# Performance work log

Hardware: AMD Instinct MI355X
Metric: run time of the kernel (lower is better)

The kernel has to match this reference:

```python
import jax, jax.numpy as jnp
import numpy as np

N, IN_DIM, HIDDEN, CLASSES, HEADS, E = 4096, 256, 512, 256, 4, 131072
HD = IN_DIM // HEADS


def setup_inputs() -> dict:
    key = jax.random.key(0)
    ks = jax.random.split(key, 16)
    s = 0.02
    x = jax.random.normal(ks[0], (N, IN_DIM), dtype=jnp.float32)
    edge_index = jax.random.randint(ks[1], (2, E), 0, N, dtype=jnp.int64)
    return {
        "x": x,
        "edge_index": edge_index,
        # GCNConv 1: in_dim -> hidden
        "gcn1_w": jax.random.normal(ks[2], (IN_DIM, HIDDEN), dtype=jnp.float32) * s,
        "gcn1_b": jnp.zeros((HIDDEN,), dtype=jnp.float32),
        # GCNConv 2: hidden -> hidden
        "gcn2_w": jax.random.normal(ks[3], (HIDDEN, HIDDEN), dtype=jnp.float32) * s,
        "gcn2_b": jnp.zeros((HIDDEN,), dtype=jnp.float32),
        # final Linear hidden -> classes
        "lin_w": jax.random.normal(ks[4], (HIDDEN, CLASSES), dtype=jnp.float32) * s,
        "lin_b": jnp.zeros((CLASSES,), dtype=jnp.float32),
        # MultiheadAttention packed in-projection (q,k,v) and out-projection
        "in_proj_w": jax.random.normal(ks[5], (3 * IN_DIM, IN_DIM), dtype=jnp.float32) * s,
        "in_proj_b": jnp.zeros((3 * IN_DIM,), dtype=jnp.float32),
        "out_proj_w": jax.random.normal(ks[6], (IN_DIM, IN_DIM), dtype=jnp.float32) * s,
        "out_proj_b": jnp.zeros((IN_DIM,), dtype=jnp.float32),
        # project: in_dim -> classes
        "proj_w": jax.random.normal(ks[7], (IN_DIM, CLASSES), dtype=jnp.float32) * s,
        "proj_b": jnp.zeros((CLASSES,), dtype=jnp.float32),
    }


def gcn_conv(x, src, dst, norm, w, b):
    # PyG GCNConv: transform, then normalized scatter-add aggregation
    h = x @ w                                   # [N+?, F] -> use gathered below
    msg = h[src] * norm[:, None]                # [E+N, F]
    out = jax.ops.segment_sum(msg, dst, num_segments=N)
    return out + b


def mha(x, in_proj_w, in_proj_b, out_proj_w, out_proj_b):
    qkv = x @ in_proj_w.T + in_proj_b           # [N, 3*IN_DIM]
    q, k, v = jnp.split(qkv, 3, axis=-1)
    # [N, IN_DIM] -> [HEADS, N, HD]
    q = q.reshape(N, HEADS, HD).transpose(1, 0, 2)
    k = k.reshape(N, HEADS, HD).transpose(1, 0, 2)
    v = v.reshape(N, HEADS, HD).transpose(1, 0, 2)
    scores = jnp.einsum("hqd,hkd->hqk", q, k) / jnp.sqrt(jnp.float32(HD))
    attn = jax.nn.softmax(scores, axis=-1)      # [HEADS, N, N]
    o = jnp.einsum("hqk,hkd->hqd", attn, v)     # [HEADS, N, HD]
    o = o.transpose(1, 0, 2).reshape(N, IN_DIM)
    return o @ out_proj_w.T + out_proj_b


def reference(x, edge_index, gcn1_w, gcn1_b, gcn2_w, gcn2_b, lin_w, lin_b,
              in_proj_w, in_proj_b, out_proj_w, out_proj_b, proj_w, proj_b):
    # --- GCN normalization with self-loops (computed once, shared by both convs) ---
    loop = jnp.arange(N, dtype=edge_index.dtype)
    src = jnp.concatenate([edge_index[0], loop])  # [E+N]
    dst = jnp.concatenate([edge_index[1], loop])
    deg = jax.ops.segment_sum(jnp.ones_like(dst, dtype=jnp.float32), dst, num_segments=N)
    dinv = jnp.where(deg > 0, jax.lax.rsqrt(deg), 0.0)
    norm = dinv[src] * dinv[dst]                  # [E+N]

    # --- GNN branch ---
    h = jax.nn.relu(gcn_conv(x, src, dst, norm, gcn1_w, gcn1_b))
    h = jax.nn.relu(gcn_conv(h, src, dst, norm, gcn2_w, gcn2_b))
    x_gnn = h @ lin_w + lin_b                     # [N, CLASSES]

    # --- Transformer branch ---
    x_tf = mha(x, in_proj_w, in_proj_b, out_proj_w, out_proj_b)
    x_proj = x_tf @ proj_w + proj_b               # [N, CLASSES]

    return jax.nn.relu(x_gnn + x_proj)
```

## Files before the change

### kernel.cpp

```cpp
#include <hip/hip_runtime.h>
#include <hip/hip_bf16.h>

#define N_NODES 4096
#define IN_DIM  256
#define HIDDEN  512
#define CLASSES 256
#define HEADS   4
#define HD      64
#define NEDGE   131072
#define NMASK   (N_NODES - 1)

typedef __attribute__((ext_vector_type(8))) short bf16x8_t;
typedef __attribute__((ext_vector_type(4))) float f32x4_t;

__device__ inline ushort f2bf(float f) {
    union { float f; uint u; } v; v.f = f;
    uint r = v.u + 0x7FFF + ((v.u >> 16) & 1);
    return (ushort)(r >> 16);
}
__device__ inline float bf2f(ushort u) {
    union { uint u; float f; } v; v.u = (uint)u << 16; return v.f;
}

__global__ void zero_i_k(int* __restrict__ p, int n) {
    int i = blockIdx.x * 256 + threadIdx.x;
    if (i < n) p[i] = 0;
}
__global__ void hist_k(const int* __restrict__ dst, int* __restrict__ cnt) {
    int i = blockIdx.x * 256 + threadIdx.x;
    if (i < NEDGE) atomicAdd(&cnt[dst[i] & NMASK], 1);
}
__global__ __launch_bounds__(256) void scan_k(const int* __restrict__ cnt,
                                              int* __restrict__ rowptr,
                                              float* __restrict__ dinv) {
    __shared__ int part[256];
    const int t = threadIdx.x;
    const int base = t * 16;
    int local[16];
    int s = 0;
    #pragma unroll
    for (int u = 0; u < 16; ++u) { local[u] = cnt[base + u]; s += local[u]; }
    part[t] = s;
    __syncthreads();
    if (t == 0) {
        int acc = 0;
        for (int i = 0; i < 256; ++i) { int v = part[i]; part[i] = acc; acc += v; }
    }
    __syncthreads();
    int acc = part[t];
    #pragma unroll
    for (int u = 0; u < 16; ++u) {
        rowptr[base + u] = acc;
        acc += local[u];
        dinv[base + u] = rsqrtf((float)local[u] + 1.0f);
    }
    if (t == 255) rowptr[N_NODES] = acc;
}
__global__ void scatter_k(const int* __restrict__ src, const int* __restrict__ dst,
                          const int* __restrict__ rowptr, int* __restrict__ tail,
                          int* __restrict__ ssrc) {
    int e = blockIdx.x * 256 + threadIdx.x;
    if (e >= NEDGE) return;
    int d = dst[e] & NMASK;
    int pos = rowptr[d] + atomicAdd(&tail[d], 1);
    ssrc[pos] = src[e] & NMASK;
}

__global__ void split_k(const float* __restrict__ in, ushort* __restrict__ hi,
                        ushort* __restrict__ lo, int n4) {
    int i = blockIdx.x * 256 + threadIdx.x;
    if (i >= n4) return;
    float4 v = ((const float4*)in)[i];
    ushort4 h, l;
    h.x = f2bf(v.x); l.x = f2bf(v.x - bf2f(h.x));
    h.y = f2bf(v.y); l.y = f2bf(v.y - bf2f(h.y));
    h.z = f2bf(v.z); l.z = f2bf(v.z - bf2f(h.z));
    h.w = f2bf(v.w); l.w = f2bf(v.w - bf2f(h.w));
    ((ushort4*)hi)[i] = h;
    ((ushort4*)lo)[i] = l;
}

__global__ __launch_bounds__(256) void tsplit_k(const float* __restrict__ W,
                                                ushort* __restrict__ th,
                                                ushort* __restrict__ tl,
                                                int K, int N) {
    __shared__ float T[64][68];
    const int k0 = blockIdx.x * 64, n0 = blockIdx.y * 64;
    const int t = threadIdx.x;
    {
        const int r = t >> 2, q = (t & 3) * 16;
        const float* src = W + (size_t)(k0 + r) * N + n0 + q;
        #pragma unroll
        for (int i = 0; i < 4; ++i)
            *(float4*)&T[r][q + i * 4] = *(const float4*)(src + i * 4);
    }
    __syncthreads();
    const int n = t >> 2, kq = (t & 3) * 16;
    ushort hh[16], ll[16];
    #pragma unroll
    for (int i = 0; i < 16; ++i) {
        float v = T[kq + i][n];
        ushort h = f2bf(v);
        hh[i] = h; ll[i] = f2bf(v - bf2f(h));
    }
    ushort* ph = th + (size_t)(n0 + n) * K + k0 + kq;
    ushort* pl = tl + (size_t)(n0 + n) * K + k0 + kq;
    #pragma unroll
    for (int i = 0; i < 16; ++i) { ph[i] = hh[i]; pl[i] = ll[i]; }
}

template<int MODE>
__global__ __launch_bounds__(256) void gemm_sp_k(
    const ushort* __restrict__ Ah, const ushort* __restrict__ Al,
    const ushort* __restrict__ Bh, const ushort* __restrict__ Bl,
    const float* __restrict__ bias, const float* src,
    void* o1, void* o2, int M, int N, int K)
{
    __shared__ ushort AsH[64][32], AsL[64][32], BsH[64][32], BsL[64][32];
    const int tid = threadIdx.x;
    const int w = tid >> 6, lane = tid & 63, g = lane >> 4, c = lane & 15;
    const int wr = w >> 1, wc = w & 1;
    const int m0 = blockIdx.x * 64, n0 = blockIdx.y * 64;
    const int sr = tid >> 2, sq = (tid & 3) * 8;

    f32x4_t acc[2][2];
    #pragma unroll
    for (int i = 0; i < 2; ++i)
        #pragma unroll
        for (int j = 0; j < 2; ++j) { acc[i][j][0]=0.f; acc[i][j][1]=0.f; acc[i][j][2]=0.f; acc[i][j][3]=0.f; }

    for (int k0 = 0; k0 < K; k0 += 32) {
        __syncthreads();
        *(bf16x8_t*)&AsH[sr][sq] = *(const bf16x8_t*)(Ah + (size_t)(m0 + sr) * K + k0 + sq);
        *(bf16x8_t*)&AsL[sr][sq] = *(const bf16x8_t*)(Al + (size_t)(m0 + sr) * K + k0 + sq);
        *(bf16x8_t*)&BsH[sr][sq] = *(const bf16x8_t*)(Bh + (size_t)(n0 + sr) * K + k0 + sq);
        *(bf16x8_t*)&BsL[sr][sq] = *(const bf16x8_t*)(Bl + (size_t)(n0 + sr) * K + k0 + sq);
        __syncthreads();

        bf16x8_t aH[2], aL[2], bH[2], bL[2];
        #pragma unroll
        for (int mr = 0; mr < 2; ++mr) {
            aH[mr] = *(const bf16x8_t*)&AsH[wr * 32 + mr * 16 + c][g * 8];
            aL[mr] = *(const bf16x8_t*)&AsL[wr * 32 + mr * 16 + c][g * 8];
        }
        #pragma unroll
        for (int nr = 0; nr < 2; ++nr) {
            bH[nr] = *(const bf16x8_t*)&BsH[wc * 32 + nr * 16 + c][g * 8];
            bL[nr] = *(const bf16x8_t*)&BsL[wc * 32 + nr * 16 + c][g * 8];
        }
        #pragma unroll
        for (int mr = 0; mr < 2; ++mr)
            #pragma unroll
            for (int nr = 0; nr < 2; ++nr) {
                acc[mr][nr] = __builtin_amdgcn_mfma_f32_16x16x32_bf16(aH[mr], bH[nr], acc[mr][nr], 0, 0, 0);
                acc[mr][nr] = __builtin_amdgcn_mfma_f32_16x16x32_bf16(aH[mr], bL[nr], acc[mr][nr], 0, 0, 0);
                acc[mr][nr] = __builtin_amdgcn_mfma_f32_16x16x32_bf16(aL[mr], bH[nr], acc[mr][nr], 0, 0, 0);
            }
    }

    #pragma unroll
    for (int mr = 0; mr < 2; ++mr)
        #pragma unroll
        for (int nr = 0; nr < 2; ++nr) {
            const int col = n0 + wc * 32 + nr * 16 + c;
            #pragma unroll
            for (int j = 0; j < 4; ++j) {
                const int row = m0 + wr * 32 + mr * 16 + g * 4 + j;
                float v = acc[mr][nr][j];
                if (MODE != 3) v += bias[col];
                if (MODE == 0) {
                    ((float*)o1)[(size_t)row * N + col] = v;
                } else if (MODE == 1) {
                    v += src[(size_t)row * N + col];
                    ((float*)o1)[(size_t)row * N + col] = fmaxf(v, 0.f);
                } else if (MODE == 2 || MODE == 3) {
                    ushort h = f2bf(v);
                    ((ushort*)o1)[(size_t)row * N + col] = h;
                    ((ushort*)o2)[(size_t)row * N + col] = f2bf(v - bf2f(h));
                } else {
                    if (col < 256) v *= 0.125f;
                    ((ushort*)o1)[(size_t)row * N + col] = f2bf(v);
                }
            }
        }
}

__global__ __launch_bounds__(256) void vtrans_k(const ushort* __restrict__ qkvb,
                                                ushort* __restrict__ vt) {
    __shared__ ushort T[64][72];
    const int n0 = blockIdx.x * 64;
    const int h  = blockIdx.y;
    const int t  = threadIdx.x;
    {
        const int r = t >> 2, q = (t & 3) * 16;
        const ushort* src = qkvb + (size_t)(n0 + r) * 768 + 512 + h * 64 + q;
        *(bf16x8_t*)&T[r][q]     = *(const bf16x8_t*)(src);
        *(bf16x8_t*)&T[r][q + 8] = *(const bf16x8_t*)(src + 8);
    }
    __syncthreads();
    const int d = t >> 2, nq = (t & 3) * 16;
    ushort tmp[16];
    #pragma unroll
    for (int i = 0; i < 16; ++i) tmp[i] = T[nq + i][d];
    ushort* dst = vt + (size_t)(h * 64 + d) * 4096 + n0 + nq;
    #pragma unroll
    for (int i = 0; i < 16; ++i) dst[i] = tmp[i];
}

__global__ __launch_bounds__(64) void attn3_k(const ushort* __restrict__ qkvb,
                                              const ushort* __restrict__ vt,
                                              float* __restrict__ po0,
                                              float* __restrict__ po1,
                                              float* __restrict__ pml)
{
    __shared__ ushort Ps[16][72];

    const int q0   = blockIdx.x * 16;
    const int h    = blockIdx.y;
    const int sp   = blockIdx.z;
    const int lane = threadIdx.x;
    const int g    = lane >> 4;
    const int c    = lane & 15;

    const ushort* qp = qkvb + (size_t)(q0 + c) * 768 + h * 64;
    const bf16x8_t qf0 = *(const bf16x8_t*)(qp + g * 8);
    const bf16x8_t qf1 = *(const bf16x8_t*)(qp + g * 8 + 32);

    f32x4_t o[4];
    float m[4], l[4];
    #pragma unroll
    for (int r = 0; r < 4; ++r) {
        m[r] = -1e30f; l[r] = 0.f;
        o[r][0] = 0.f; o[r][1] = 0.f; o[r][2] = 0.f; o[r][3] = 0.f;
    }

    const ushort* kcol = qkvb + 256 + h * 64 + g * 8;
    const ushort* vrow = vt + (size_t)(h * 64 + c) * 4096 + g * 8;

    for (int kt = sp * 32; kt < sp * 32 + 32; ++kt) {
        const int kv0 = kt * 64;

        f32x4_t s[4];
        #pragma unroll
        for (int t = 0; t < 4; ++t) {
            const ushort* kr = kcol + (size_t)(kv0 + c + 16 * t) * 768;
            bf16x8_t b0 = *(const bf16x8_t*)(kr);
            bf16x8_t b1 = *(const bf16x8_t*)(kr + 32);
            f32x4_t a; a[0] = 0.f; a[1] = 0.f; a[2] = 0.f; a[3] = 0.f;
            a = __builtin_amdgcn_mfma_f32_16x16x32_bf16(qf0, b0, a, 0, 0, 0);
            a = __builtin_amdgcn_mfma_f32_16x16x32_bf16(qf1, b1, a, 0, 0, 0);
            s[t] = a;
        }

        bf16x8_t vf[4][2];
        #pragma unroll
        for (int d0 = 0; d0 < 4; ++d0) {
            const ushort* vr = vrow + (size_t)(16 * d0) * 4096 + kv0;
            vf[d0][0] = *(const bf16x8_t*)(vr);
            vf[d0][1] = *(const bf16x8_t*)(vr + 32);
        }

        #pragma unroll
        for (int r = 0; r < 4; ++r) {
            float mx = fmaxf(fmaxf(s[0][r], s[1][r]), fmaxf(s[2][r], s[3][r]));
            mx = fmaxf(mx, __shfl_xor(mx, 1));
            mx = fmaxf(mx, __shfl_xor(mx, 2));
            mx = fmaxf(mx, __shfl_xor(mx, 4));
            mx = fmaxf(mx, __shfl_xor(mx, 8));
            float mn = fmaxf(m[r], mx);
            float alpha = __expf(m[r] - mn);
            m[r] = mn;
            float p0 = __expf(s[0][r] - mn);
            float p1 = __expf(s[1][r] - mn);
            float p2 = __expf(s[2][r] - mn);
            float p3 = __expf(s[3][r] - mn);
            float sum = p0 + p1 + p2 + p3;
            sum += __shfl_xor(sum, 1);
            sum += __shfl_xor(sum, 2);
            sum += __shfl_xor(sum, 4);
            sum += __shfl_xor(sum, 8);
            l[r] = l[r] * alpha + sum;
            o[0][r] *= alpha; o[1][r] *= alpha; o[2][r] *= alpha; o[3][r] *= alpha;
            ushort* pr = &Ps[g * 4 + r][c];
            pr[0]  = f2bf(p0);
            pr[16] = f2bf(p1);
            pr[32] = f2bf(p2);
            pr[48] = f2bf(p3);
        }

        bf16x8_t pa0 = *(const bf16x8_t*)&Ps[c][g * 8];
        bf16x8_t pa1 = *(const bf16x8_t*)&Ps[c][g * 8 + 32];
        #pragma unroll
        for (int d0 = 0; d0 < 4; ++d0) {
            o[d0] = __builtin_amdgcn_mfma_f32_16x16x32_bf16(pa0, vf[d0][0], o[d0], 0, 0, 0);
            o[d0] = __builtin_amdgcn_mfma_f32_16x16x32_bf16(pa1, vf[d0][1], o[d0], 0, 0, 0);
        }
    }

    float* po = sp ? po1 : po0;
    #pragma unroll
    for (int r = 0; r < 4; ++r) {
        float* op = po + ((size_t)h * 4096 + q0 + g * 4 + r) * 64 + c;
        #pragma unroll
        for (int d0 = 0; d0 < 4; ++d0)
            op[16 * d0] = o[d0][r];
    }
    if (c == 0) {
        #pragma unroll
        for (int r = 0; r < 4; ++r) {
            size_t idx = ((size_t)(sp * 4 + h) * 4096 + q0 + g * 4 + r) * 2;
            pml[idx]     = m[r];
            pml[idx + 1] = l[r];
        }
    }
}

__global__ __launch_bounds__(256) void comb_k(const float* __restrict__ po0,
                                              const float* __restrict__ po1,
                                              const float* __restrict__ pml,
                                              ushort* __restrict__ aoh,
                                              ushort* __restrict__ aol)
{
    int idx = blockIdx.x * 256 + threadIdx.x;
    int row = idx >> 4;
    int h = row >> 12, q = row & 4095;
    int dq = (idx & 15) * 4;
    const float* a = pml + ((size_t)(0 * 4 + h) * 4096 + q) * 2;
    const float* b = pml + ((size_t)(1 * 4 + h) * 4096 + q) * 2;
    float m1 = a[0], l1 = a[1], m2 = b[0], l2 = b[1];
    float mw = fmaxf(m1, m2);
    float a1 = __expf(m1 - mw), a2 = __expf(m2 - mw);
    float inv = 1.0f / (a1 * l1 + a2 * l2);
    float4 o1 = *(const float4*)(po0 + (size_t)row * 64 + dq);
    float4 o2 = *(const float4*)(po1 + (size_t)row * 64 + dq);
    float vx = (a1 * o1.x + a2 * o2.x) * inv;
    float vy = (a1 * o1.y + a2 * o2.y) * inv;
    float vz = (a1 * o1.z + a2 * o2.z) * inv;
    float vw = (a1 * o1.w + a2 * o2.w) * inv;
    size_t oi = (size_t)q * 256 + h * 64 + dq;
    ushort4 H, L;
    H.x = f2bf(vx); L.x = f2bf(vx - bf2f(H.x));
    H.y = f2bf(vy); L.y = f2bf(vy - bf2f(H.y));
    H.z = f2bf(vz); L.z = f2bf(vz - bf2f(H.z));
    H.w = f2bf(vw); L.w = f2bf(vw - bf2f(H.w));
    *(ushort4*)(aoh + oi) = H;
    *(ushort4*)(aol + oi) = L;
}

__global__ __launch_bounds__(128) void csr_agg2_k(const ushort* __restrict__ hh,
                                                  const ushort* __restrict__ hl,
                                                  const int* __restrict__ rowptr,
                                                  const int* __restrict__ ssrc,
                                                  const float* __restrict__ dinv,
                                                  const float* __restrict__ bias,
                                                  ushort* __restrict__ oh,
                                                  ushort* __restrict__ ol) {
    __shared__ int   nbr[64];
    __shared__ float wnb[64];
    const int d = blockIdx.x;
    const int c = threadIdx.x;
    const int beg = rowptr[d], end = rowptr[d + 1];

    float4 acc = {0.f, 0.f, 0.f, 0.f};
    for (int j0 = beg; j0 < end; j0 += 64) {
        const int mcnt = min(64, end - j0);
        if (c < mcnt) {
            int s = ssrc[j0 + c];
            nbr[c] = s;
            wnb[c] = dinv[s];
        }
        __syncthreads();
        for (int u = 0; u < mcnt; ++u) {
            const int s = nbr[u];
            const float w = wnb[u];
            ushort4 vh = *(const ushort4*)(hh + (size_t)s * 512 + c * 4);
            ushort4 vl = *(const ushort4*)(hl + (size_t)s * 512 + c * 4);
            acc.x += w * (bf2f(vh.x) + bf2f(vl.x));
            acc.y += w * (bf2f(vh.y) + bf2f(vl.y));
            acc.z += w * (bf2f(vh.z) + bf2f(vl.z));
            acc.w += w * (bf2f(vh.w) + bf2f(vl.w));
        }
        __syncthreads();
    }

    const float wd = dinv[d];
    const float wd2 = wd * wd;
    ushort4 sh = *(const ushort4*)(hh + (size_t)d * 512 + c * 4);
    ushort4 sl = *(const ushort4*)(hl + (size_t)d * 512 + c * 4);
    float4 bv = *((const float4*)bias + c);
    float r0 = fmaxf(acc.x * wd + wd2 * (bf2f(sh.x) + bf2f(sl.x)) + bv.x, 0.f);
    float r1 = fmaxf(acc.y * wd + wd2 * (bf2f(sh.y) + bf2f(sl.y)) + bv.y, 0.f);
    float r2 = fmaxf(acc.z * wd + wd2 * (bf2f(sh.z) + bf2f(sl.z)) + bv.z, 0.f);
    float r3 = fmaxf(acc.w * wd + wd2 * (bf2f(sh.w) + bf2f(sl.w)) + bv.w, 0.f);
    ushort4 H, L;
    H.x = f2bf(r0); L.x = f2bf(r0 - bf2f(H.x));
    H.y = f2bf(r1); L.y = f2bf(r1 - bf2f(H.y));
    H.z = f2bf(r2); L.z = f2bf(r2 - bf2f(H.z));
    H.w = f2bf(r3); L.w = f2bf(r3 - bf2f(H.w));
    *(ushort4*)(oh + (size_t)d * 512 + c * 4) = H;
    *(ushort4*)(ol + (size_t)d * 512 + c * 4) = L;
}

extern "C" void kernel_launch(void* const* d_in, const int* in_sizes, int n_in,
                              void* d_out, int out_size, void* d_ws, size_t ws_size,
                              hipStream_t stream)
{
    const float* x          = (const float*)d_in[0];
    const int*   eidx       = (const int*)d_in[1];
    const float* gcn1_w     = (const float*)d_in[2];
    const float* gcn1_b     = (const float*)d_in[3];
    const float* gcn2_w     = (const float*)d_in[4];
    const float* gcn2_b     = (const float*)d_in[5];
    const float* lin_w      = (const float*)d_in[6];
    const float* lin_b      = (const float*)d_in[7];
    const float* in_proj_w  = (const float*)d_in[8];
    const float* in_proj_b  = (const float*)d_in[9];
    const float* out_proj_w = (const float*)d_in[10];
    const float* out_proj_b = (const float*)d_in[11];
    const float* proj_w     = (const float*)d_in[12];
    const float* proj_b     = (const float*)d_in[13];
    float* out = (float*)d_out;

    const int* esrc = eidx;
    const int* edst = eidx + NEDGE;

    char* base = (char*)d_ws;
    size_t off = 0;
    auto take = [&](size_t bytes) -> char* {
        char* p = base + off;
        off = (off + bytes + 255) & ~(size_t)255;
        return p;
    };

    int*   cnt    = (int*)take(N_NODES * 4);
    int*   tail   = (int*)take(N_NODES * 4);
    int*   rowptr = (int*)take((N_NODES + 8) * 4);
    int*   ssrc   = (int*)take(NEDGE * 4);
    float* dinv   = (float*)take(N_NODES * 4);
    float* pml    = (float*)take(2 * HEADS * N_NODES * 2 * 4);

    ushort* wreg = (ushort*)take(2 * 1024 * 1024);
    ushort* ipW_h = wreg;
    ushort* ipW_l = ipW_h + 768 * 256;
    ushort* opW_h = ipW_l + 768 * 256;
    ushort* opW_l = opW_h + 256 * 256;
    ushort* pjT_h = opW_l + 256 * 256;
    ushort* pjT_l = pjT_h + 256 * 256;
    ushort* g1T_h = wreg;
    ushort* g1T_l = g1T_h + 512 * 256;
    ushort* g2T_h = g1T_l + 512 * 256;
    ushort* g2T_l = g2T_h + 512 * 512;
    ushort* lT_h  = g2T_l + 512 * 512;
    ushort* lT_l  = lT_h + 256 * 512;

    ushort* xs_h = (ushort*)take(N_NODES * IN_DIM * 2);
    ushort* xs_l = (ushort*)take(N_NODES * IN_DIM * 2);

    char* R2 = take(8 * 1024 * 1024);
    ushort* qkvb = (ushort*)R2;
    ushort* vt   = qkvb + (size_t)N_NODES * 768;
    ushort* Ph   = (ushort*)R2;
    ushort* Pl   = Ph + (size_t)N_NODES * HIDDEN;

    char* R3 = take(8 * 1024 * 1024);
    ushort* ao_h = (ushort*)R3;
    ushort* ao_l = ao_h + (size_t)N_NODES * IN_DIM;
    ushort* xt_h = ao_l + (size_t)N_NODES * IN_DIM;
    ushort* xt_l = xt_h + (size_t)N_NODES * IN_DIM;
    ushort* Qh   = (ushort*)R3;
    ushort* Ql   = Qh + (size_t)N_NODES * HIDDEN;

    float* po0 = out;
    float* po1 = (float*)xt_h;

    zero_i_k<<<(2 * N_NODES + 255) / 256, 256, 0, stream>>>(cnt, 2 * N_NODES);
    hist_k<<<(NEDGE + 255) / 256, 256, 0, stream>>>(edst, cnt);
    scan_k<<<1, 256, 0, stream>>>(cnt, rowptr, dinv);
    scatter_k<<<(NEDGE + 255) / 256, 256, 0, stream>>>(esrc, edst, rowptr, tail, ssrc);

    split_k<<<(N_NODES * IN_DIM / 4 + 255) / 256, 256, 0, stream>>>(x, xs_h, xs_l, N_NODES * IN_DIM / 4);
    split_k<<<(768 * 256 / 4 + 255) / 256, 256, 0, stream>>>(in_proj_w, ipW_h, ipW_l, 768 * 256 / 4);
    split_k<<<(256 * 256 / 4 + 255) / 256, 256, 0, stream>>>(out_proj_w, opW_h, opW_l, 256 * 256 / 4);
    tsplit_k<<<dim3(4, 4), 256, 0, stream>>>(proj_w, pjT_h, pjT_l, 256, 256);

    gemm_sp_k<4><<<dim3(64, 12), 256, 0, stream>>>(xs_h, xs_l, ipW_h, ipW_l,
        in_proj_b, nullptr, qkvb, nullptr, N_NODES, 768, 256);
    vtrans_k<<<dim3(64, 4), 256, 0, stream>>>(qkvb, vt);
    attn3_k<<<dim3(256, 4, 2), 64, 0, stream>>>(qkvb, vt, po0, po1, pml);
    comb_k<<<(HEADS * N_NODES * 16) / 256, 256, 0, stream>>>(po0, po1, pml, ao_h, ao_l);
    gemm_sp_k<2><<<dim3(64, 4), 256, 0, stream>>>(ao_h, ao_l, opW_h, opW_l,
        out_proj_b, nullptr, xt_h, xt_l, N_NODES, 256, 256);
    gemm_sp_k<0><<<dim3(64, 4), 256, 0, stream>>>(xt_h, xt_l, pjT_h, pjT_l,
        proj_b, nullptr, out, nullptr, N_NODES, 256, 256);

    tsplit_k<<<dim3(4, 8), 256, 0, stream>>>(gcn1_w, g1T_h, g1T_l, 256, 512);
    tsplit_k<<<dim3(8, 8), 256, 0, stream>>>(gcn2_w, g2T_h, g2T_l, 512, 512);
    tsplit_k<<<dim3(8, 4), 256, 0, stream>>>(lin_w, lT_h, lT_l, 512, 256);

    gemm_sp_k<3><<<dim3(64, 8), 256, 0, stream>>>(xs_h, xs_l, g1T_h, g1T_l,
        nullptr, nullptr, Ph, Pl, N_NODES, HIDDEN, IN_DIM);
    csr_agg2_k<<<N_NODES, 128, 0, stream>>>(Ph, Pl, rowptr, ssrc, dinv, gcn1_b, Qh, Ql);
    gemm_sp_k<3><<<dim3(64, 8), 256, 0, stream>>>(Qh, Ql, g2T_h, g2T_l,
        nullptr, nullptr, Ph, Pl, N_NODES, HIDDEN, HIDDEN);
    csr_agg2_k<<<N_NODES, 128, 0, stream>>>(Ph, Pl, rowptr, ssrc, dinv, gcn2_b, Qh, Ql);

    gemm_sp_k<1><<<dim3(64, 4), 256, 0, stream>>>(Qh, Ql, lT_h, lT_l,
        lin_b, out, out, nullptr, N_NODES, CLASSES, HIDDEN);
}
```

Before: 375.7 us.

## Split attention KV range three ways with register double-buffered K prefetch

The flash-attention kernel now splits the 64 KV tiles into three chunks instead of two. That raises the block count for more parallelism across CUs, and a three-way combine kernel merges the partial results. Inside the loop, K fragments for the next tile are loaded into a second register set while the current tile is computed, so global load latency is hidden. Intermediate buffers are remapped to hold the third partial output. The cost is more registers per thread, tempered by a launch_bounds occupancy hint, plus extra combine traffic.

After: 378.2 us. Within noise of the previous version (+0.7%).

```diff
diff --git a/kernel.cpp b/kernel.cpp
--- a/kernel.cpp
+++ b/kernel.cpp
@@ -207,17 +207,88 @@
     for (int i = 0; i < 16; ++i) dst[i] = tmp[i];
 }
 
-__global__ __launch_bounds__(64) void attn3_k(const ushort* __restrict__ qkvb,
-                                              const ushort* __restrict__ vt,
-                                              float* __restrict__ po0,
-                                              float* __restrict__ po1,
-                                              float* __restrict__ pml)
+#define PF_K(KB, KTIDX)                                                        \
+    {                                                                          \
+        const int kk = (KTIDX);                                                \
+        const size_t b = (size_t)(kk * 64 + c) * 768;                          \
+        KB[0][0] = *(const bf16x8_t*)(kcol + b);                               \
+        KB[0][1] = *(const bf16x8_t*)(kcol + b + 32);                          \
+        KB[1][0] = *(const bf16x8_t*)(kcol + b + 16 * 768);                    \
+        KB[1][1] = *(const bf16x8_t*)(kcol + b + 16 * 768 + 32);               \
+        KB[2][0] = *(const bf16x8_t*)(kcol + b + 32 * 768);                    \
+        KB[2][1] = *(const bf16x8_t*)(kcol + b + 32 * 768 + 32);               \
+        KB[3][0] = *(const bf16x8_t*)(kcol + b + 48 * 768);                    \
+        KB[3][1] = *(const bf16x8_t*)(kcol + b + 48 * 768 + 32);               \
+    }
+
+#define ATTN_TILE(KB, KT)                                                      \
+    {                                                                          \
+        const int kv0 = (KT) * 64;                                             \
+        bf16x8_t vf[4][2];                                                     \
+        _Pragma("unroll")                                                      \
+        for (int d0 = 0; d0 < 4; ++d0) {                                       \
+            const ushort* vr = vrow + (size_t)(16 * d0) * 4096 + kv0;          \
+            vf[d0][0] = *(const bf16x8_t*)(vr);                                \
+            vf[d0][1] = *(const bf16x8_t*)(vr + 32);                           \
+        }                                                                      \
+        f32x4_t s[4];                                                          \
+        _Pragma("unroll")                                                      \
+        for (int t = 0; t < 4; ++t) {                                          \
+            f32x4_t a; a[0] = 0.f; a[1] = 0.f; a[2] = 0.f; a[3] = 0.f;         \
+            a = __builtin_amdgcn_mfma_f32_16x16x32_bf16(qf0, KB[t][0], a, 0, 0, 0); \
+            a = __builtin_amdgcn_mfma_f32_16x16x32_bf16(qf1, KB[t][1], a, 0, 0, 0); \
+            s[t] = a;                                                          \
+        }                                                                      \
+        _Pragma("unroll")                                                      \
+        for (int r = 0; r < 4; ++r) {                                          \
+            float mx = fmaxf(fmaxf(s[0][r], s[1][r]), fmaxf(s[2][r], s[3][r]));\
+            mx = fmaxf(mx, __shfl_xor(mx, 1));                                 \
+            mx = fmaxf(mx, __shfl_xor(mx, 2));                                 \
+            mx = fmaxf(mx, __shfl_xor(mx, 4));                                 \
+            mx = fmaxf(mx, __shfl_xor(mx, 8));                                 \
+            float mn = fmaxf(m[r], mx);                                        \
+            float alpha = __expf(m[r] - mn);                                   \
+            m[r] = mn;                                                         \
+            float p0 = __expf(s[0][r] - mn);                                   \
+            float p1 = __expf(s[1][r] - mn);                                   \
+            float p2 = __expf(s[2][r] - mn);                                   \
+            float p3 = __expf(s[3][r] - mn);                                   \
+            float sum = p0 + p1 + p2 + p3;                                     \
+            sum += __shfl_xor(sum, 1);                                         \
+            sum += __shfl_xor(sum, 2);                                         \
+            sum += __shfl_xor(sum, 4);                                         \
+            sum += __shfl_xor(sum, 8);                                         \
+            l[r] = l[r] * alpha + sum;                                         \
+            o[0][r] *= alpha; o[1][r] *= alpha; o[2][r] *= alpha; o[3][r] *= alpha; \
+            ushort* pr = &Ps[g * 4 + r][c];                                    \
+            pr[0]  = f2bf(p0);                                                 \
+            pr[16] = f2bf(p1);                                                 \
+            pr[32] = f2bf(p2);                                                 \
+            pr[48] = f2bf(p3);                                                 \
+        }                                                                      \
+        bf16x8_t pa0 = *(const bf16x8_t*)&Ps[c][g * 8];                        \
+        bf16x8_t pa1 = *(const bf16x8_t*)&Ps[c][g * 8 + 32];                   \
+        _Pragma("unroll")                                                      \
+        for (int d0 = 0; d0 < 4; ++d0) {                                       \
+            o[d0] = __builtin_amdgcn_mfma_f32_16x16x32_bf16(pa0, vf[d0][0], o[d0], 0, 0, 0); \
+            o[d0] = __builtin_amdgcn_mfma_f32_16x16x32_bf16(pa1, vf[d0][1], o[d0], 0, 0, 0); \
+        }                                                                      \
+    }
+
+__global__ __launch_bounds__(64, 3) void attn4_k(const ushort* __restrict__ qkvb,
+                                                 const ushort* __restrict__ vt,
+                                                 float* __restrict__ po0,
+                                                 float* __restrict__ po1,
+                                                 float* __restrict__ po2,
+                                                 float* __restrict__ pml)
 {
     __shared__ ushort Ps[16][72];
 
     const int q0   = blockIdx.x * 16;
     const int h    = blockIdx.y;
     const int sp   = blockIdx.z;
+    const int kt_beg = sp * 22;
+    const int kt_end = min(64, kt_beg + 22);
     const int lane = threadIdx.x;
     const int g    = lane >> 4;
     const int c    = lane & 15;
@@ -237,67 +308,23 @@
     const ushort* kcol = qkvb + 256 + h * 64 + g * 8;
     const ushort* vrow = vt + (size_t)(h * 64 + c) * 4096 + g * 8;
 
-    for (int kt = sp * 32; kt < sp * 32 + 32; ++kt) {
-        const int kv0 = kt * 64;
-
-        f32x4_t s[4];
-        #pragma unroll
-        for (int t = 0; t < 4; ++t) {
-            const ushort* kr = kcol + (size_t)(kv0 + c + 16 * t) * 768;
-            bf16x8_t b0 = *(const bf16x8_t*)(kr);
-            bf16x8_t b1 = *(const bf16x8_t*)(kr + 32);
-            f32x4_t a; a[0] = 0.f; a[1] = 0.f; a[2] = 0.f; a[3] = 0.f;
-            a = __builtin_amdgcn_mfma_f32_16x16x32_bf16(qf0, b0, a, 0, 0, 0);
-            a = __builtin_amdgcn_mfma_f32_16x16x32_bf16(qf1, b1, a, 0, 0, 0);
-            s[t] = a;
-        }
-
-        bf16x8_t vf[4][2];
-        #pragma unroll
-        for (int d0 = 0; d0 < 4; ++d0) {
-            const ushort* vr = vrow + (size_t)(16 * d0) * 4096 + kv0;
-            vf[d0][0] = *(const bf16x8_t*)(vr);
-            vf[d0][1] = *(const bf16x8_t*)(vr + 32);
-        }
-
-        #pragma unroll
-        for (int r = 0; r < 4; ++r) {
-            float mx = fmaxf(fmaxf(s[0][r], s[1][r]), fmaxf(s[2][r], s[3][r]));
-            mx = fmaxf(mx, __shfl_xor(mx, 1));
-            mx = fmaxf(mx, __shfl_xor(mx, 2));
-            mx = fmaxf(mx, __shfl_xor(mx, 4));
-            mx = fmaxf(mx, __shfl_xor(mx, 8));
-            float mn = fmaxf(m[r], mx);
-            float alpha = __expf(m[r] - mn);
-            m[r] = mn;
-            float p0 = __expf(s[0][r] - mn);
-            float p1 = __expf(s[1][r] - mn);
-            float p2 = __expf(s[2][r] - mn);
-            float p3 = __expf(s[3][r] - mn);
-            float sum = p0 + p1 + p2 + p3;
-            sum += __shfl_xor(sum, 1);
-            sum += __shfl_xor(sum, 2);
-            sum += __shfl_xor(sum, 4);
-            sum += __shfl_xor(sum, 8);
-            l[r] = l[r] * alpha + sum;
-            o[0][r] *= alpha; o[1][r] *= alpha; o[2][r] *= alpha; o[3][r] *= alpha;
-            ushort* pr = &Ps[g * 4 + r][c];
-            pr[0]  = f2bf(p0);
-            pr[16] = f2bf(p1);
-            pr[32] = f2bf(p2);
-            pr[48] = f2bf(p3);
-        }
-
-        bf16x8_t pa0 = *(const bf16x8_t*)&Ps[c][g * 8];
-        bf16x8_t pa1 = *(const bf16x8_t*)&Ps[c][g * 8 + 32];
-        #pragma unroll
-        for (int d0 = 0; d0 < 4; ++d0) {
-            o[d0] = __builtin_amdgcn_mfma_f32_16x16x32_bf16(pa0, vf[d0][0], o[d0], 0, 0, 0);
-            o[d0] = __builtin_amdgcn_mfma_f32_16x16x32_bf16(pa1, vf[d0][1], o[d0], 0, 0, 0);
-        }
-    }
-
-    float* po = sp ? po1 : po0;
+    bf16x8_t kbA[4][2], kbB[4][2];
+    PF_K(kbA, kt_beg)
+
+    for (int kt = kt_beg; kt < kt_end; kt += 2) {
+        {
+            const int ktn = kt + 1;
+            PF_K(kbB, ktn)
+        }
+        ATTN_TILE(kbA, kt)
+        {
+            const int ktn2 = min(kt + 2, kt_end - 1);
+            PF_K(kbA, ktn2)
+        }
+        ATTN_TILE(kbB, kt + 1)
+    }
+
+    float* po = (sp == 0) ? po0 : (sp == 1) ? po1 : po2;
     #pragma unroll
     for (int r = 0; r < 4; ++r) {
         float* op = po + ((size_t)h * 4096 + q0 + g * 4 + r) * 64 + c;
@@ -315,11 +342,12 @@
     }
 }
 
-__global__ __launch_bounds__(256) void comb_k(const float* __restrict__ po0,
-                                              const float* __restrict__ po1,
-                                              const float* __restrict__ pml,
-                                              ushort* __restrict__ aoh,
-                                              ushort* __restrict__ aol)
+__global__ __launch_bounds__(256) void comb3_k(const float* __restrict__ po0,
+                                               const float* __restrict__ po1,
+                                               const float* __restrict__ po2,
+                                               const float* __restrict__ pml,
+                                               ushort* __restrict__ aoh,
+                                               ushort* __restrict__ aol)
 {
     int idx = blockIdx.x * 256 + threadIdx.x;
     int row = idx >> 4;
@@ -327,16 +355,18 @@
     int dq = (idx & 15) * 4;
     const float* a = pml + ((size_t)(0 * 4 + h) * 4096 + q) * 2;
     const float* b = pml + ((size_t)(1 * 4 + h) * 4096 + q) * 2;
-    float m1 = a[0], l1 = a[1], m2 = b[0], l2 = b[1];
-    float mw = fmaxf(m1, m2);
-    float a1 = __expf(m1 - mw), a2 = __expf(m2 - mw);
-    float inv = 1.0f / (a1 * l1 + a2 * l2);
-    float4 o1 = *(const float4*)(po0 + (size_t)row * 64 + dq);
-    float4 o2 = *(const float4*)(po1 + (size_t)row * 64 + dq);
-    float vx = (a1 * o1.x + a2 * o2.x) * inv;
-    float vy = (a1 * o1.y + a2 * o2.y) * inv;
-    float vz = (a1 * o1.z + a2 * o2.z) * inv;
-    float vw = (a1 * o1.w + a2 * o2.w) * inv;
+    const float* e = pml + ((size_t)(2 * 4 + h) * 4096 + q) * 2;
+    float m0 = a[0], l0 = a[1], m1 = b[0], l1 = b[1], m2 = e[0], l2 = e[1];
+    float mw = fmaxf(fmaxf(m0, m1), m2);
+    float a0 = __expf(m0 - mw), a1 = __expf(m1 - mw), a2 = __expf(m2 - mw);
+    float inv = 1.0f / (a0 * l0 + a1 * l1 + a2 * l2);
+    float4 o0 = *(const float4*)(po0 + (size_t)row * 64 + dq);
+    float4 o1 = *(const float4*)(po1 + (size_t)row * 64 + dq);
+    float4 o2 = *(const float4*)(po2 + (size_t)row * 64 + dq);
+    float vx = (a0 * o0.x + a1 * o1.x + a2 * o2.x) * inv;
+    float vy = (a0 * o0.y + a1 * o1.y + a2 * o2.y) * inv;
+    float vz = (a0 * o0.z + a1 * o1.z + a2 * o2.z) * inv;
+    float vw = (a0 * o0.w + a1 * o1.w + a2 * o2.w) * inv;
     size_t oi = (size_t)q * 256 + h * 64 + dq;
     ushort4 H, L;
     H.x = f2bf(vx); L.x = f2bf(vx - bf2f(H.x));
@@ -437,7 +467,7 @@
     int*   rowptr = (int*)take((N_NODES + 8) * 4);
     int*   ssrc   = (int*)take(NEDGE * 4);
     float* dinv   = (float*)take(N_NODES * 4);
-    float* pml    = (float*)take(2 * HEADS * N_NODES * 2 * 4);
+    float* pml    = (float*)take(3 * HEADS * N_NODES * 2 * 4);
 
     ushort* wreg = (ushort*)take(2 * 1024 * 1024);
     ushort* ipW_h = wreg;
@@ -459,19 +489,20 @@
     char* R2 = take(8 * 1024 * 1024);
     ushort* qkvb = (ushort*)R2;
     ushort* vt   = qkvb + (size_t)N_NODES * 768;
+    ushort* ao_h = (ushort*)R2;
+    ushort* ao_l = ao_h + (size_t)N_NODES * IN_DIM;
     ushort* Ph   = (ushort*)R2;
     ushort* Pl   = Ph + (size_t)N_NODES * HIDDEN;
 
     char* R3 = take(8 * 1024 * 1024);
-    ushort* ao_h = (ushort*)R3;
-    ushort* ao_l = ao_h + (size_t)N_NODES * IN_DIM;
-    ushort* xt_h = ao_l + (size_t)N_NODES * IN_DIM;
+    float* po1 = (float*)R3;
+    float* po2 = (float*)(R3 + 4 * 1024 * 1024);
+    ushort* xt_h = (ushort*)R3;
     ushort* xt_l = xt_h + (size_t)N_NODES * IN_DIM;
     ushort* Qh   = (ushort*)R3;
     ushort* Ql   = Qh + (size_t)N_NODES * HIDDEN;
 
     float* po0 = out;
-    float* po1 = (float*)xt_h;
 
     zero_i_k<<<(2 * N_NODES + 255) / 256, 256, 0, stream>>>(cnt, 2 * N_NODES);
     hist_k<<<(NEDGE + 255) / 256, 256, 0, stream>>>(edst, cnt);
@@ -486,8 +517,8 @@
     gemm_sp_k<4><<<dim3(64, 12), 256, 0, stream>>>(xs_h, xs_l, ipW_h, ipW_l,
         in_proj_b, nullptr, qkvb, nullptr, N_NODES, 768, 256);
     vtrans_k<<<dim3(64, 4), 256, 0, stream>>>(qkvb, vt);
-    attn3_k<<<dim3(256, 4, 2), 64, 0, stream>>>(qkvb, vt, po0, po1, pml);
-    comb_k<<<(HEADS * N_NODES * 16) / 256, 256, 0, stream>>>(po0, po1, pml, ao_h, ao_l);
+    attn4_k<<<dim3(256, 4, 3), 64, 0, stream>>>(qkvb, vt, po0, po1, po2, pml);
+    comb3_k<<<(HEADS * N_NODES * 16) / 256, 256, 0, stream>>>(po0, po1, po2, pml, ao_h, ao_l);
     gemm_sp_k<2><<<dim3(64, 4), 256, 0, stream>>>(ao_h, ao_l, opW_h, opW_l,
         out_proj_b, nullptr, xt_h, xt_l, N_NODES, 256, 256);
     gemm_sp_k<0><<<dim3(64, 4), 256, 0, stream>>>(xt_h, xt_l, pjT_h, pjT_l,
```
